# Kernel tuning notes

Hardware: AMD Instinct MI355X
Metric: run time of the kernel (lower is better)

## Reference

```python
import jax, jax.numpy as jnp
import numpy as np

NZ, NX = 512, 512        # domain_shape
NT = 1200                # time steps
NSRC = 4                 # number of point sources
NREC = 512               # number of receivers
DT = 1e-3                # time step (s)
DH = 10.0                # grid spacing (m)


def setup_inputs() -> dict:
    key = jax.random.key(0)
    k1, k2, k3, k4, k5, k6 = jax.random.split(key, 6)
    x = jax.random.normal(k1, (NSRC, NT), dtype=jnp.float32)          # source wavelets
    vel = 1500.0 + 1000.0 * jax.random.uniform(k2, (NZ, NX), dtype=jnp.float32)  # velocity model (learned param)
    src_z = jax.random.randint(k3, (NSRC,), 2, 500)
    src_x = jax.random.randint(k4, (NSRC,), 2, 500)
    rec_z = jax.random.randint(k5, (NREC,), 2, 500)
    rec_x = jax.random.randint(k6, (NREC,), 2, 500)
    return {"x": x, "vel": vel, "src_z": src_z, "src_x": src_x,
            "rec_z": rec_z, "rec_x": rec_x}


def _laplacian(u, dh):
    # 5-point stencil with zero (Dirichlet) boundary
    up = jnp.pad(u, 1)
    return (up[:-2, 1:-1] + up[2:, 1:-1] + up[1:-1, :-2] + up[1:-1, 2:]
            - 4.0 * u) / (dh * dh)


def reference(x, vel, src_z, src_x, rec_z, rec_x):
    # 2nd-order acoustic wave equation time-marching (WaveRNN forward):
    #   h_new = 2*h1 - h2 + (v*dt)^2 * lap(h1) + source injection
    # followed by receiver probing each step.
    c2dt2 = (vel * DT) ** 2  # [NZ, NX]

    def step(carry, amp):
        h1, h2 = carry
        h_new = 2.0 * h1 - h2 + c2dt2 * _laplacian(h1, DH)
        h_new = h_new.at[src_z, src_x].add(amp)     # scatter source injection
        rec = h_new[rec_z, rec_x]                   # gather receiver probe
        return (h_new, h1), rec

    h0 = jnp.zeros((NZ, NX), dtype=x.dtype)
    _, traces = jax.lax.scan(step, (h0, h0), x.T)   # traces: [NT, NREC]
    y = traces[:, :, None]                          # [NT, NREC, n_recv_types=1]
    return y
```

## Files before the change

kernel.cpp:

```cpp
#include <hip/hip_runtime.h>
#include <hip/hip_cooperative_groups.h>

namespace cg = cooperative_groups;

#define NZg  512
#define NXg  512
#define NT   1200
#define NSRC 4
#define NREC 512
#define DTC  0.001f
#define DHC  10.0f

#define TILE   32
#define KK     16
#define EE     64
#define EEP    (EE + 2)
#define NBATCH 75
#define NTH    512

typedef unsigned long long u64;

__device__ __forceinline__ u64 ld_agent(const u64* p) {
    return __hip_atomic_load(p, __ATOMIC_RELAXED, __HIP_MEMORY_SCOPE_AGENT);
}
__device__ __forceinline__ void st_agent(u64* p, u64 v) {
    __hip_atomic_store(p, v, __ATOMIC_RELAXED, __HIP_MEMORY_SCOPE_AGENT);
}
__device__ __forceinline__ u64 pack2(float a, float b) {
    union { float f[2]; u64 u; } c; c.f[0] = a; c.f[1] = b; return c.u;
}
__device__ __forceinline__ float2 unpack2(u64 v) {
    union { u64 u; float f[2]; } c; c.u = v; return make_float2(c.f[0], c.f[1]);
}

__global__ __launch_bounds__(NTH, 1)
void wave_p42(const float* __restrict__ xsrc,
              const float* __restrict__ vel,
              const int*   __restrict__ src_z,
              const int*   __restrict__ src_x,
              const int*   __restrict__ rec_z,
              const int*   __restrict__ rec_x,
              float*       __restrict__ out,
              u64*         __restrict__ slot0,
              u64*         __restrict__ slot1,
              int*         __restrict__ flags)
{
    cg::grid_group grid = cg::this_grid();

    __shared__ float sA[EEP * EE];
    __shared__ float sB[EEP * EE];
    __shared__ float sx[NSRC * NT];
    __shared__ int   recl[NREC];
    __shared__ int   nrec_s;

    const int tid = threadIdx.x;
    const int me  = blockIdx.x;
    const int bz  = me >> 4, bx = me & 15;
    const int oz  = bz * TILE - KK;
    const int ox  = bx * TILE - KK;
    const int pc  = tid & 15;
    const int pr  = tid >> 4;
    const int lx  = 4 * pc;
    const int z0  = 2 * pr;
    const int gx  = ox + lx;
    const int gz0 = oz + z0;
    const int gz1 = gz0 + 1;

    if (tid == 0) { flags[me] = 0; nrec_s = 0; }

    if (tid < 2 * EE) {
        const int r = (tid < EE) ? 0 : (EEP - 1);
        const int c = tid & (EE - 1);
        sA[r * EE + c] = 0.f;  sB[r * EE + c] = 0.f;
    }
    for (int i = tid; i < NSRC * NT; i += NTH) sx[i] = xsrc[i];
    __syncthreads();

    for (int r = tid; r < NREC; r += NTH) {
        const int rz = rec_z[r], rx = rec_x[r];
        if (rz >= bz * TILE && rz < bz * TILE + TILE &&
            rx >= bx * TILE && rx < bx * TILE + TILE) {
            const int lzp = rz - oz + 1;
            const int lxx = rx - ox;
            const int s = atomicAdd(&nrec_s, 1);
            recl[s] = (r << 16) | (lzp << 8) | lxx;
        }
    }

    float4 c0 = make_float4(0.f, 0.f, 0.f, 0.f);
    float4 c1 = c0;
    unsigned int smask = 0;
    {
        int szr[NSRC], sxr[NSRC];
#pragma unroll
        for (int s = 0; s < NSRC; ++s) { szr[s] = src_z[s]; sxr[s] = src_x[s]; }
        float* cc0 = &c0.x;  float* cc1 = &c1.x;
#pragma unroll
        for (int k = 0; k < 4; ++k) {
            const int gxk = gx + k;
            const bool okx = (gxk >= 0 && gxk < NXg);
            if (okx && gz0 >= 0 && gz0 < NZg) {
                const float v = vel[gz0 * NXg + gxk];
                cc0[k] = (v * DTC) * (v * DTC) / (DHC * DHC);
#pragma unroll
                for (int s = 0; s < NSRC; ++s)
                    if (szr[s] == gz0 && sxr[s] == gxk) smask |= 1u << (k * 4 + s);
            }
            if (okx && gz1 >= 0 && gz1 < NZg) {
                const float v = vel[gz1 * NXg + gxk];
                cc1[k] = (v * DTC) * (v * DTC) / (DHC * DHC);
#pragma unroll
                for (int s = 0; s < NSRC; ++s)
                    if (szr[s] == gz1 && sxr[s] == gxk) smask |= 1u << ((4 + k) * 4 + s);
            }
        }
    }
    __syncthreads();
    grid.sync();

    float4 own0, own1, prv0, prv1;
    const int cb0 = (z0 + 1) * EE + lx;
    const int cb1 = cb0 + EE;

    bool havenb = false; int nbidx = 0;
    if (tid < 9 && tid != 4) {
        const int nz = bz + tid / 3 - 1, nx = bx + tid % 3 - 1;
        havenb = (nz >= 0 && nz < 16 && nx >= 0 && nx < 16);
        nbidx  = nz * 16 + nx;
    }

    auto STEP = [&](float* __restrict__ dst_, const float* __restrict__ src_,
                    int t) {
        const float4 U  = *(const float4*)&src_[cb0 - EE];
        const float4 D  = *(const float4*)&src_[cb1 + EE];
        const float  l0 = src_[cb0 - 1], r0v = src_[cb0 + 4];
        const float  l1 = src_[cb1 - 1], r1v = src_[cb1 + 4];

        float4 n0, n1;
        n0.x = 2.f * own0.x - prv0.x + c0.x * (U.x + own1.x + l0     + own0.y - 4.f * own0.x);
        n0.y = 2.f * own0.y - prv0.y + c0.y * (U.y + own1.y + own0.x + own0.z - 4.f * own0.y);
        n0.z = 2.f * own0.z - prv0.z + c0.z * (U.z + own1.z + own0.y + own0.w - 4.f * own0.z);
        n0.w = 2.f * own0.w - prv0.w + c0.w * (U.w + own1.w + own0.z + r0v    - 4.f * own0.w);
        n1.x = 2.f * own1.x - prv1.x + c1.x * (own0.x + D.x + l1     + own1.y - 4.f * own1.x);
        n1.y = 2.f * own1.y - prv1.y + c1.y * (own0.y + D.y + own1.x + own1.z - 4.f * own1.y);
        n1.z = 2.f * own1.z - prv1.z + c1.z * (own0.z + D.z + own1.y + own1.w - 4.f * own1.z);
        n1.w = 2.f * own1.w - prv1.w + c1.w * (own0.w + D.w + own1.z + r1v    - 4.f * own1.w);

        if (smask) {
            float* pn0 = &n0.x;  float* pn1 = &n1.x;
#pragma unroll
            for (int s = 0; s < NSRC; ++s) {
                const float amp = sx[s * NT + t];
#pragma unroll
                for (int k = 0; k < 4; ++k) {
                    if (smask & (1u << (k * 4 + s)))       pn0[k] += amp;
                    if (smask & (1u << ((4 + k) * 4 + s))) pn1[k] += amp;
                }
            }
        }

        *(float4*)&dst_[cb0] = n0;
        *(float4*)&dst_[cb1] = n1;
        prv0 = own0;  prv1 = own1;
        own0 = n0;    own1 = n1;
        __syncthreads();
        for (int r = tid; r < nrec_s; r += NTH) {
            const int e = recl[r];
            out[t * NREC + (e >> 16)] = dst_[((e >> 8) & 0xFF) * EE + (e & 0xFF)];
        }
    };

    for (int b = 0; b < NBATCH; ++b) {
        const u64* gin  = (b & 1) ? slot1 : slot0;
        u64*       gout = (b & 1) ? slot0 : slot1;

        if (b > 0) {
            if (havenb) {
                while (__hip_atomic_load(&flags[nbidx], __ATOMIC_RELAXED,
                                         __HIP_MEMORY_SCOPE_AGENT) < b)
                    __builtin_amdgcn_s_sleep(1);
            }
            __syncthreads();
        }

        {
            float* po0 = &own0.x;  float* pp0 = &prv0.x;
            float* po1 = &own1.x;  float* pp1 = &prv1.x;
#pragma unroll
            for (int k = 0; k < 4; ++k) {
                const int gxk = gx + k;
                const bool okx = (gxk >= 0 && gxk < NXg);
                if (b > 0 && okx && gz0 >= 0 && gz0 < NZg) {
                    const float2 v = unpack2(ld_agent(&gin[gz0 * NXg + gxk]));
                    po0[k] = v.x;  pp0[k] = v.y;
                } else { po0[k] = 0.f;  pp0[k] = 0.f; }
                if (b > 0 && okx && gz1 >= 0 && gz1 < NZg) {
                    const float2 v = unpack2(ld_agent(&gin[gz1 * NXg + gxk]));
                    po1[k] = v.x;  pp1[k] = v.y;
                } else { po1[k] = 0.f;  pp1[k] = 0.f; }
            }
        }
        *(float4*)&sB[cb0] = own0;
        *(float4*)&sB[cb1] = own1;
        __syncthreads();

        for (int j = 0; j < KK; j += 2) {
            STEP(sA, sB, b * KK + j);
            STEP(sB, sA, b * KK + j + 1);
        }

        if (pr >= 8 && pr < 24 && pc >= 4 && pc < 12) {
            const float* po0 = &own0.x;  const float* pp0 = &prv0.x;
            const float* po1 = &own1.x;  const float* pp1 = &prv1.x;
#pragma unroll
            for (int k = 0; k < 4; ++k) {
                st_agent(&gout[gz0 * NXg + gx + k], pack2(po0[k], pp0[k]));
                st_agent(&gout[gz1 * NXg + gx + k], pack2(po1[k], pp1[k]));
            }
        }
        __syncthreads();
        if (tid == 0) {
            __hip_atomic_store(&flags[me], b + 1, __ATOMIC_RELAXED,
                               __HIP_MEMORY_SCOPE_AGENT);
        }
    }
}

extern "C" void kernel_launch(void* const* d_in, const int* in_sizes, int n_in,
                              void* d_out, int out_size, void* d_ws, size_t ws_size,
                              hipStream_t stream) {
    const float* xsrc  = (const float*)d_in[0];
    const float* vel   = (const float*)d_in[1];
    const int*   src_z = (const int*)  d_in[2];
    const int*   src_x = (const int*)  d_in[3];
    const int*   rec_z = (const int*)  d_in[4];
    const int*   rec_x = (const int*)  d_in[5];
    float*       out   = (float*)d_out;

    u64* slot0 = (u64*)d_ws;
    u64* slot1 = slot0 + NZg * NXg;
    int* flags = (int*)(slot1 + NZg * NXg);

    void* args[] = {(void*)&xsrc, (void*)&vel, (void*)&src_z, (void*)&src_x,
                    (void*)&rec_z, (void*)&rec_x, (void*)&out,
                    (void*)&slot0, (void*)&slot1, (void*)&flags};

    dim3 grid(256), block(NTH);
    hipLaunchCooperativeKernel((const void*)wave_p42, grid, block, args, 0, stream);
}
```

Baseline: 899.5 us.

## Keep inner tile state in registers, wave-level neighbor wait, buffer receiver writes

```diff
diff --git a/kernel.cpp b/kernel.cpp
--- a/kernel.cpp
+++ b/kernel.cpp
@@ -17,6 +17,7 @@
 #define EEP    (EE + 2)
 #define NBATCH 75
 #define NTH    512
+#define RBUFN  32
 
 typedef unsigned long long u64;
 
@@ -26,6 +27,9 @@
 __device__ __forceinline__ void st_agent(u64* p, u64 v) {
     __hip_atomic_store(p, v, __ATOMIC_RELAXED, __HIP_MEMORY_SCOPE_AGENT);
 }
+__device__ __forceinline__ int ld_flag(const int* p) {
+    return __hip_atomic_load(p, __ATOMIC_RELAXED, __HIP_MEMORY_SCOPE_AGENT);
+}
 __device__ __forceinline__ u64 pack2(float a, float b) {
     union { float f[2]; u64 u; } c; c.f[0] = a; c.f[1] = b; return c.u;
 }
@@ -34,39 +38,43 @@
 }
 
 __global__ __launch_bounds__(NTH, 1)
-void wave_p42(const float* __restrict__ xsrc,
-              const float* __restrict__ vel,
-              const int*   __restrict__ src_z,
-              const int*   __restrict__ src_x,
-              const int*   __restrict__ rec_z,
-              const int*   __restrict__ rec_x,
-              float*       __restrict__ out,
-              u64*         __restrict__ slot0,
-              u64*         __restrict__ slot1,
-              int*         __restrict__ flags)
+void wave_lt(const float* __restrict__ xsrc,
+             const float* __restrict__ vel,
+             const int*   __restrict__ src_z,
+             const int*   __restrict__ src_x,
+             const int*   __restrict__ rec_z,
+             const int*   __restrict__ rec_x,
+             float*       __restrict__ out,
+             u64*         __restrict__ slot0,
+             u64*         __restrict__ slot1,
+             int*         __restrict__ flags)
 {
     cg::grid_group grid = cg::this_grid();
 
     __shared__ float sA[EEP * EE];
     __shared__ float sB[EEP * EE];
     __shared__ float sx[NSRC * NT];
+    __shared__ float rbuf[RBUFN * KK];
     __shared__ int   recl[NREC];
     __shared__ int   nrec_s;
-
-    const int tid = threadIdx.x;
-    const int me  = blockIdx.x;
-    const int bz  = me >> 4, bx = me & 15;
-    const int oz  = bz * TILE - KK;
-    const int ox  = bx * TILE - KK;
-    const int pc  = tid & 15;
-    const int pr  = tid >> 4;
-    const int lx  = 4 * pc;
-    const int z0  = 2 * pr;
-    const int gx  = ox + lx;
-    const int gz0 = oz + z0;
-    const int gz1 = gz0 + 1;
-
-    if (tid == 0) { flags[me] = 0; nrec_s = 0; }
+    __shared__ int   sdone;
+
+    const int tid  = threadIdx.x;
+    const int lane = tid & 63;
+    const int me   = blockIdx.x;
+    const int bz   = me >> 4, bx = me & 15;
+    const int oz   = bz * TILE - KK;
+    const int ox   = bx * TILE - KK;
+    const int pc   = tid & 15;
+    const int pr   = tid >> 4;
+    const int lx   = 4 * pc;
+    const int z0   = 2 * pr;
+    const int gx   = ox + lx;
+    const int gz0  = oz + z0;
+    const int gz1  = gz0 + 1;
+    const bool inner = (pr >= 8 && pr < 24 && pc >= 4 && pc < 12);
+
+    if (tid == 0) { flags[me] = 0; nrec_s = 0; sdone = 0; }
 
     if (tid < 2 * EE) {
         const int r = (tid < EE) ? 0 : (EEP - 1);
@@ -116,21 +124,24 @@
         }
     }
     __syncthreads();
+    const int nr    = nrec_s;
+    const int myrec = (tid < nr) ? recl[tid] : 0;
     grid.sync();
 
-    float4 own0, own1, prv0, prv1;
+    float4 own0 = make_float4(0.f, 0.f, 0.f, 0.f), own1 = own0;
+    float4 prv0 = own0, prv1 = own0;
     const int cb0 = (z0 + 1) * EE + lx;
     const int cb1 = cb0 + EE;
 
     bool havenb = false; int nbidx = 0;
-    if (tid < 9 && tid != 4) {
-        const int nz = bz + tid / 3 - 1, nx = bx + tid % 3 - 1;
+    if (lane < 9 && lane != 4) {
+        const int nz = bz + lane / 3 - 1, nx = bx + lane % 3 - 1;
         havenb = (nz >= 0 && nz < 16 && nx >= 0 && nx < 16);
         nbidx  = nz * 16 + nx;
     }
 
     auto STEP = [&](float* __restrict__ dst_, const float* __restrict__ src_,
-                    int t) {
+                    int t, int jj) {
         const float4 U  = *(const float4*)&src_[cb0 - EE];
         const float4 D  = *(const float4*)&src_[cb1 + EE];
         const float  l0 = src_[cb0 - 1], r0v = src_[cb0 + 4];
@@ -164,9 +175,10 @@
         prv0 = own0;  prv1 = own1;
         own0 = n0;    own1 = n1;
         __syncthreads();
-        for (int r = tid; r < nrec_s; r += NTH) {
-            const int e = recl[r];
-            out[t * NREC + (e >> 16)] = dst_[((e >> 8) & 0xFF) * EE + (e & 0xFF)];
+        if (tid < nr) {
+            const float v = dst_[((myrec >> 8) & 0xFF) * EE + (myrec & 0xFF)];
+            if (tid < RBUFN) rbuf[tid * KK + jj] = v;
+            else out[t * NREC + (myrec >> 16)] = v;
         }
     };
 
@@ -175,15 +187,24 @@
         u64*       gout = (b & 1) ? slot0 : slot1;
 
         if (b > 0) {
-            if (havenb) {
-                while (__hip_atomic_load(&flags[nbidx], __ATOMIC_RELAXED,
-                                         __HIP_MEMORY_SCOPE_AGENT) < b)
+            bool rel = (__hip_atomic_load(&sdone, __ATOMIC_RELAXED,
+                                          __HIP_MEMORY_SCOPE_WORKGROUP) >= b);
+            while (!rel) {
+                const bool ok = havenb ? (ld_flag(&flags[nbidx]) >= b) : true;
+                if (__all(ok)) {
+                    if (lane == 0)
+                        __hip_atomic_store(&sdone, b, __ATOMIC_RELAXED,
+                                           __HIP_MEMORY_SCOPE_WORKGROUP);
+                    rel = true;
+                } else {
                     __builtin_amdgcn_s_sleep(1);
-            }
-            __syncthreads();
-        }
-
-        {
+                    rel = (__hip_atomic_load(&sdone, __ATOMIC_RELAXED,
+                                             __HIP_MEMORY_SCOPE_WORKGROUP) >= b);
+                }
+            }
+        }
+
+        if (!inner) {
             float* po0 = &own0.x;  float* pp0 = &prv0.x;
             float* po1 = &own1.x;  float* pp1 = &prv1.x;
 #pragma unroll
@@ -205,11 +226,18 @@
         __syncthreads();
 
         for (int j = 0; j < KK; j += 2) {
-            STEP(sA, sB, b * KK + j);
-            STEP(sB, sA, b * KK + j + 1);
-        }
-
-        if (pr >= 8 && pr < 24 && pc >= 4 && pc < 12) {
+            STEP(sA, sB, b * KK + j,     j);
+            STEP(sB, sA, b * KK + j + 1, j + 1);
+        }
+
+        if (tid < nr && tid < RBUFN) {
+            const int rid = myrec >> 16;
+#pragma unroll
+            for (int j = 0; j < KK; ++j)
+                out[(b * KK + j) * NREC + rid] = rbuf[tid * KK + j];
+        }
+
+        if (inner) {
             const float* po0 = &own0.x;  const float* pp0 = &prv0.x;
             const float* po1 = &own1.x;  const float* pp1 = &prv1.x;
 #pragma unroll
@@ -246,5 +274,5 @@
                     (void*)&slot0, (void*)&slot1, (void*)&flags};
 
     dim3 grid(256), block(NTH);
-    hipLaunchCooperativeKernel((const void*)wave_p42, grid, block, args, 0, stream);
-}
+    hipLaunchCooperativeKernel((const void*)wave_lt, grid, block, args, 0, stream);
+}
```

Measured after the change: 934.4 us. 1.04x slower.

## Split grid into 512 half-height tiles, two blocks per CU, three rows per thread

Applied to the files above, without the earlier changes.

```diff
diff --git a/kernel.cpp b/kernel.cpp
--- a/kernel.cpp
+++ b/kernel.cpp
@@ -11,12 +11,17 @@
 #define DTC  0.001f
 #define DHC  10.0f
 
-#define TILE   32
+#define TZ     16
+#define TX     32
 #define KK     16
-#define EE     64
-#define EEP    (EE + 2)
+#define EZ     48
+#define EX     64
+#define EZP    50
 #define NBATCH 75
-#define NTH    512
+#define NTH    256
+#define NBZ    32
+#define NBX    16
+#define NBLK   512
 
 typedef unsigned long long u64;
 
@@ -33,8 +38,8 @@
     union { u64 u; float f[2]; } c; c.u = v; return make_float2(c.f[0], c.f[1]);
 }
 
-__global__ __launch_bounds__(NTH, 1)
-void wave_p42(const float* __restrict__ xsrc,
+__global__ __launch_bounds__(NTH, 2)
+void wave_tlp(const float* __restrict__ xsrc,
               const float* __restrict__ vel,
               const int*   __restrict__ src_z,
               const int*   __restrict__ src_x,
@@ -47,8 +52,8 @@
 {
     cg::grid_group grid = cg::this_grid();
 
-    __shared__ float sA[EEP * EE];
-    __shared__ float sB[EEP * EE];
+    __shared__ float sA[EZP * EX];
+    __shared__ float sB[EZP * EX];
     __shared__ float sx[NSRC * NT];
     __shared__ int   recl[NREC];
     __shared__ int   nrec_s;
@@ -56,30 +61,29 @@
     const int tid = threadIdx.x;
     const int me  = blockIdx.x;
     const int bz  = me >> 4, bx = me & 15;
-    const int oz  = bz * TILE - KK;
-    const int ox  = bx * TILE - KK;
+    const int oz  = bz * TZ - KK;
+    const int ox  = bx * TX - KK;
     const int pc  = tid & 15;
     const int pr  = tid >> 4;
     const int lx  = 4 * pc;
-    const int z0  = 2 * pr;
+    const int z0  = 3 * pr;
     const int gx  = ox + lx;
     const int gz0 = oz + z0;
-    const int gz1 = gz0 + 1;
 
     if (tid == 0) { flags[me] = 0; nrec_s = 0; }
 
-    if (tid < 2 * EE) {
-        const int r = (tid < EE) ? 0 : (EEP - 1);
-        const int c = tid & (EE - 1);
-        sA[r * EE + c] = 0.f;  sB[r * EE + c] = 0.f;
+    if (tid < 2 * EX) {
+        const int r = (tid < EX) ? 0 : (EZP - 1);
+        const int c = tid & (EX - 1);
+        sA[r * EX + c] = 0.f;  sB[r * EX + c] = 0.f;
     }
     for (int i = tid; i < NSRC * NT; i += NTH) sx[i] = xsrc[i];
     __syncthreads();
 
     for (int r = tid; r < NREC; r += NTH) {
         const int rz = rec_z[r], rx = rec_x[r];
-        if (rz >= bz * TILE && rz < bz * TILE + TILE &&
-            rx >= bx * TILE && rx < bx * TILE + TILE) {
+        if (rz >= bz * TZ && rz < bz * TZ + TZ &&
+            rx >= bx * TX && rx < bx * TX + TX) {
             const int lzp = rz - oz + 1;
             const int lxx = rx - ox;
             const int s = atomicAdd(&nrec_s, 1);
@@ -88,85 +92,93 @@
     }
 
     float4 c0 = make_float4(0.f, 0.f, 0.f, 0.f);
-    float4 c1 = c0;
-    unsigned int smask = 0;
+    float4 c1 = c0, c2 = c0;
+    u64 smask = 0ull;
     {
         int szr[NSRC], sxr[NSRC];
 #pragma unroll
         for (int s = 0; s < NSRC; ++s) { szr[s] = src_z[s]; sxr[s] = src_x[s]; }
-        float* cc0 = &c0.x;  float* cc1 = &c1.x;
-#pragma unroll
-        for (int k = 0; k < 4; ++k) {
-            const int gxk = gx + k;
-            const bool okx = (gxk >= 0 && gxk < NXg);
-            if (okx && gz0 >= 0 && gz0 < NZg) {
-                const float v = vel[gz0 * NXg + gxk];
-                cc0[k] = (v * DTC) * (v * DTC) / (DHC * DHC);
-#pragma unroll
-                for (int s = 0; s < NSRC; ++s)
-                    if (szr[s] == gz0 && sxr[s] == gxk) smask |= 1u << (k * 4 + s);
-            }
-            if (okx && gz1 >= 0 && gz1 < NZg) {
-                const float v = vel[gz1 * NXg + gxk];
-                cc1[k] = (v * DTC) * (v * DTC) / (DHC * DHC);
-#pragma unroll
-                for (int s = 0; s < NSRC; ++s)
-                    if (szr[s] == gz1 && sxr[s] == gxk) smask |= 1u << ((4 + k) * 4 + s);
+        float* cc[3] = {&c0.x, &c1.x, &c2.x};
+#pragma unroll
+        for (int i = 0; i < 3; ++i) {
+            const int gz = gz0 + i;
+            const bool okz = (gz >= 0 && gz < NZg);
+#pragma unroll
+            for (int k = 0; k < 4; ++k) {
+                const int gxk = gx + k;
+                if (okz && gxk >= 0 && gxk < NXg) {
+                    const float v = vel[gz * NXg + gxk];
+                    cc[i][k] = (v * DTC) * (v * DTC) / (DHC * DHC);
+#pragma unroll
+                    for (int s = 0; s < NSRC; ++s)
+                        if (szr[s] == gz && sxr[s] == gxk)
+                            smask |= 1ull << ((i * 4 + k) * 4 + s);
+                }
             }
         }
     }
     __syncthreads();
     grid.sync();
 
-    float4 own0, own1, prv0, prv1;
-    const int cb0 = (z0 + 1) * EE + lx;
-    const int cb1 = cb0 + EE;
+    float4 own0, own1, own2, prv0, prv1, prv2;
+    const int cb0 = (z0 + 1) * EX + lx;
+    const int cb1 = cb0 + EX;
+    const int cb2 = cb1 + EX;
 
     bool havenb = false; int nbidx = 0;
     if (tid < 9 && tid != 4) {
         const int nz = bz + tid / 3 - 1, nx = bx + tid % 3 - 1;
-        havenb = (nz >= 0 && nz < 16 && nx >= 0 && nx < 16);
-        nbidx  = nz * 16 + nx;
+        havenb = (nz >= 0 && nz < NBZ && nx >= 0 && nx < NBX);
+        nbidx  = nz * NBX + nx;
     }
 
     auto STEP = [&](float* __restrict__ dst_, const float* __restrict__ src_,
                     int t) {
-        const float4 U  = *(const float4*)&src_[cb0 - EE];
-        const float4 D  = *(const float4*)&src_[cb1 + EE];
+        const float4 U  = *(const float4*)&src_[cb0 - EX];
+        const float4 D  = *(const float4*)&src_[cb2 + EX];
         const float  l0 = src_[cb0 - 1], r0v = src_[cb0 + 4];
         const float  l1 = src_[cb1 - 1], r1v = src_[cb1 + 4];
-
-        float4 n0, n1;
+        const float  l2 = src_[cb2 - 1], r2v = src_[cb2 + 4];
+
+        float4 n0, n1, n2;
         n0.x = 2.f * own0.x - prv0.x + c0.x * (U.x + own1.x + l0     + own0.y - 4.f * own0.x);
         n0.y = 2.f * own0.y - prv0.y + c0.y * (U.y + own1.y + own0.x + own0.z - 4.f * own0.y);
         n0.z = 2.f * own0.z - prv0.z + c0.z * (U.z + own1.z + own0.y + own0.w - 4.f * own0.z);
         n0.w = 2.f * own0.w - prv0.w + c0.w * (U.w + own1.w + own0.z + r0v    - 4.f * own0.w);
-        n1.x = 2.f * own1.x - prv1.x + c1.x * (own0.x + D.x + l1     + own1.y - 4.f * own1.x);
-        n1.y = 2.f * own1.y - prv1.y + c1.y * (own0.y + D.y + own1.x + own1.z - 4.f * own1.y);
-        n1.z = 2.f * own1.z - prv1.z + c1.z * (own0.z + D.z + own1.y + own1.w - 4.f * own1.z);
-        n1.w = 2.f * own1.w - prv1.w + c1.w * (own0.w + D.w + own1.z + r1v    - 4.f * own1.w);
+
+        n1.x = 2.f * own1.x - prv1.x + c1.x * (own0.x + own2.x + l1     + own1.y - 4.f * own1.x);
+        n1.y = 2.f * own1.y - prv1.y + c1.y * (own0.y + own2.y + own1.x + own1.z - 4.f * own1.y);
+        n1.z = 2.f * own1.z - prv1.z + c1.z * (own0.z + own2.z + own1.y + own1.w - 4.f * own1.z);
+        n1.w = 2.f * own1.w - prv1.w + c1.w * (own0.w + own2.w + own1.z + r1v    - 4.f * own1.w);
+
+        n2.x = 2.f * own2.x - prv2.x + c2.x * (own1.x + D.x + l2     + own2.y - 4.f * own2.x);
+        n2.y = 2.f * own2.y - prv2.y + c2.y * (own1.y + D.y + own2.x + own2.z - 4.f * own2.y);
+        n2.z = 2.f * own2.z - prv2.z + c2.z * (own1.z + D.z + own2.y + own2.w - 4.f * own2.z);
+        n2.w = 2.f * own2.w - prv2.w + c2.w * (own1.w + D.w + own2.z + r2v    - 4.f * own2.w);
 
         if (smask) {
-            float* pn0 = &n0.x;  float* pn1 = &n1.x;
+            float* pn[3] = {&n0.x, &n1.x, &n2.x};
 #pragma unroll
             for (int s = 0; s < NSRC; ++s) {
                 const float amp = sx[s * NT + t];
 #pragma unroll
-                for (int k = 0; k < 4; ++k) {
-                    if (smask & (1u << (k * 4 + s)))       pn0[k] += amp;
-                    if (smask & (1u << ((4 + k) * 4 + s))) pn1[k] += amp;
-                }
+                for (int i = 0; i < 3; ++i)
+#pragma unroll
+                    for (int k = 0; k < 4; ++k)
+                        if (smask & (1ull << ((i * 4 + k) * 4 + s)))
+                            pn[i][k] += amp;
             }
         }
 
         *(float4*)&dst_[cb0] = n0;
         *(float4*)&dst_[cb1] = n1;
-        prv0 = own0;  prv1 = own1;
-        own0 = n0;    own1 = n1;
+        *(float4*)&dst_[cb2] = n2;
+        prv0 = own0;  prv1 = own1;  prv2 = own2;
+        own0 = n0;    own1 = n1;    own2 = n2;
         __syncthreads();
         for (int r = tid; r < nrec_s; r += NTH) {
             const int e = recl[r];
-            out[t * NREC + (e >> 16)] = dst_[((e >> 8) & 0xFF) * EE + (e & 0xFF)];
+            out[t * NREC + (e >> 16)] = dst_[((e >> 8) & 0xFF) * EX + (e & 0xFF)];
         }
     };
 
@@ -184,24 +196,25 @@
         }
 
         {
-            float* po0 = &own0.x;  float* pp0 = &prv0.x;
-            float* po1 = &own1.x;  float* pp1 = &prv1.x;
-#pragma unroll
-            for (int k = 0; k < 4; ++k) {
-                const int gxk = gx + k;
-                const bool okx = (gxk >= 0 && gxk < NXg);
-                if (b > 0 && okx && gz0 >= 0 && gz0 < NZg) {
-                    const float2 v = unpack2(ld_agent(&gin[gz0 * NXg + gxk]));
-                    po0[k] = v.x;  pp0[k] = v.y;
-                } else { po0[k] = 0.f;  pp0[k] = 0.f; }
-                if (b > 0 && okx && gz1 >= 0 && gz1 < NZg) {
-                    const float2 v = unpack2(ld_agent(&gin[gz1 * NXg + gxk]));
-                    po1[k] = v.x;  pp1[k] = v.y;
-                } else { po1[k] = 0.f;  pp1[k] = 0.f; }
+            float* po[3] = {&own0.x, &own1.x, &own2.x};
+            float* pp[3] = {&prv0.x, &prv1.x, &prv2.x};
+#pragma unroll
+            for (int i = 0; i < 3; ++i) {
+                const int gz = gz0 + i;
+                const bool okz = (gz >= 0 && gz < NZg);
+#pragma unroll
+                for (int k = 0; k < 4; ++k) {
+                    const int gxk = gx + k;
+                    if (b > 0 && okz && gxk >= 0 && gxk < NXg) {
+                        const float2 v = unpack2(ld_agent(&gin[gz * NXg + gxk]));
+                        po[i][k] = v.x;  pp[i][k] = v.y;
+                    } else { po[i][k] = 0.f;  pp[i][k] = 0.f; }
+                }
             }
         }
         *(float4*)&sB[cb0] = own0;
         *(float4*)&sB[cb1] = own1;
+        *(float4*)&sB[cb2] = own2;
         __syncthreads();
 
         for (int j = 0; j < KK; j += 2) {
@@ -209,13 +222,19 @@
             STEP(sB, sA, b * KK + j + 1);
         }
 
-        if (pr >= 8 && pr < 24 && pc >= 4 && pc < 12) {
-            const float* po0 = &own0.x;  const float* pp0 = &prv0.x;
-            const float* po1 = &own1.x;  const float* pp1 = &prv1.x;
-#pragma unroll
-            for (int k = 0; k < 4; ++k) {
-                st_agent(&gout[gz0 * NXg + gx + k], pack2(po0[k], pp0[k]));
-                st_agent(&gout[gz1 * NXg + gx + k], pack2(po1[k], pp1[k]));
+        if (pc >= 4 && pc < 12) {
+            const float* po[3] = {&own0.x, &own1.x, &own2.x};
+            const float* pp[3] = {&prv0.x, &prv1.x, &prv2.x};
+#pragma unroll
+            for (int i = 0; i < 3; ++i) {
+                const int lz = z0 + i;
+                if (lz >= KK && lz < KK + TZ) {
+                    const int gz = oz + lz;
+#pragma unroll
+                    for (int k = 0; k < 4; ++k)
+                        st_agent(&gout[gz * NXg + gx + k],
+                                 pack2(po[i][k], pp[i][k]));
+                }
             }
         }
         __syncthreads();
@@ -245,6 +264,6 @@
                     (void*)&rec_z, (void*)&rec_x, (void*)&out,
                     (void*)&slot0, (void*)&slot1, (void*)&flags};
 
-    dim3 grid(256), block(NTH);
-    hipLaunchCooperativeKernel((const void*)wave_p42, grid, block, args, 0, stream);
-}
+    dim3 grid(NBLK), block(NTH);
+    hipLaunchCooperativeKernel((const void*)wave_tlp, grid, block, args, 0, stream);
+}
```

After: 1.086 ms. 20.7% more time.
